# Kernel optimization log

Measured on AMD Instinct MI355X. Metric: run time of the kernel, lower is better.

The kernel has to match this reference:

```python
import jax, jax.numpy as jnp
import numpy as np
from jax import lax

B, L, D, H = 2, 4096, 1024, 16
K = 4            # short conv kernel size
HD = D // H      # head dim = 64
EPS = 1e-5


def causal_dw_conv(x, w):
    # depthwise causal conv: x [B,L,D], w [D,K]
    xp = jnp.pad(x, ((0, 0), (K - 1, 0), (0, 0)))
    out = xp[:, 0:L, :] * w[:, 0]
    for j in range(1, K):
        out = out + xp[:, j:j + L, :] * w[:, j]
    return out


def setup_inputs() -> dict:
    key = jax.random.key(0)
    ks = jax.random.split(key, 10)
    s = 0.02
    return {
        "hidden_states": jax.random.normal(ks[0], (B, L, D), jnp.float32),
        "Wq": jax.random.normal(ks[1], (D, D), jnp.float32) * s,
        "Wk": jax.random.normal(ks[2], (D, D), jnp.float32) * s,
        "Wv": jax.random.normal(ks[3], (D, D), jnp.float32) * s,
        "Wb": jax.random.normal(ks[4], (D, H), jnp.float32) * s,
        "conv_q": jax.random.normal(ks[5], (D, K), jnp.float32) * s,
        "conv_k": jax.random.normal(ks[6], (D, K), jnp.float32) * s,
        "conv_v": jax.random.normal(ks[7], (D, K), jnp.float32) * s,
        "o_norm_w": jnp.ones((HD,), jnp.float32),
        "Wo": jax.random.normal(ks[8], (D, D), jnp.float32) * s,
    }


def reference(hidden_states, Wq, Wk, Wv, Wb, conv_q, conv_k, conv_v, o_norm_w, Wo):
    x = hidden_states
    # projections + short causal conv with SiLU (qk_activation == 'silu')
    q = jax.nn.silu(causal_dw_conv(x @ Wq, conv_q))
    k = jax.nn.silu(causal_dw_conv(x @ Wk, conv_k))
    v = jax.nn.silu(causal_dw_conv(x @ Wv, conv_v))

    # [B,L,D] -> [L,B,H,hd] for the time scan
    def to_heads(t):
        return t.reshape(B, L, H, HD).transpose(1, 0, 2, 3)

    q, k, v = to_heads(q), to_heads(k), to_heads(v)

    # l2 qk-norm
    q = q / jnp.linalg.norm(q, axis=-1, keepdims=True)
    k = k / jnp.linalg.norm(k, axis=-1, keepdims=True)

    # beta gate [L,B,H]
    beta = jax.nn.sigmoid(x @ Wb).transpose(1, 0, 2)

    def step(S, inp):
        qt, kt, vt, bt = inp  # [B,H,hd] x3, [B,H]
        v_old = jnp.einsum('bhk,bhkv->bhv', kt, S)
        delta = (vt - v_old) * bt[..., None]
        S = S + jnp.einsum('bhk,bhv->bhkv', kt, delta)
        ot = jnp.einsum('bhk,bhkv->bhv', qt, S)
        return S, ot

    S0 = jnp.zeros((B, H, HD, HD), x.dtype)
    _, o = lax.scan(step, S0, (q, k, v, beta))  # o: [L,B,H,hd]
    o = o.transpose(1, 0, 2, 3)  # [B,L,H,hd]

    # per-head RMSNorm
    rms = jax.lax.rsqrt(jnp.mean(o * o, axis=-1, keepdims=True) + EPS)
    o = o * rms * o_norm_w

    return o.reshape(B, L, D) @ Wo
```

## Files before the change

kernel.cpp:

```cpp
#include <hip/hip_runtime.h>
#include <hip/hip_bf16.h>
#include <math.h>

#define BB 2
#define LL 4096
#define DD 1024
#define HH 16
#define HDIM 64
#define CC 64
#define NC 64
#define BH 32
#define GG 8
#define GS 8

typedef __attribute__((ext_vector_type(8))) short short8;
typedef __attribute__((ext_vector_type(4))) float f32x4;
typedef unsigned short u16;
typedef unsigned int u32;

__device__ __forceinline__ u16 f2bf(float f) {
    unsigned int u = __float_as_uint(f);
    unsigned int r = (u + 0x7fffu + ((u >> 16) & 1u)) >> 16;
    return (u16)r;
}
__device__ __forceinline__ float bf2f(u16 h) {
    return __uint_as_float((unsigned)h << 16);
}
__device__ __forceinline__ void split2(float x, u16& h, u16& l) {
    h = f2bf(x);
    l = f2bf(x - bf2f(h));
}
__device__ __forceinline__ u32 packhl(float x) {
    u16 h, l; split2(x, h, l);
    return (u32)h | ((u32)l << 16);
}
__device__ __forceinline__ float unpackhl(u32 v) {
    return bf2f((u16)v) + bf2f((u16)(v >> 16));
}
__device__ __forceinline__ float4 ld_bf4(const u16* p) {
    uint2 v = *(const uint2*)p;
    return make_float4(bf2f((u16)v.x), bf2f((u16)(v.x >> 16)),
                       bf2f((u16)v.y), bf2f((u16)(v.y >> 16)));
}

__device__ __forceinline__ void gld_lds16(const void* g, void* l) {
    __builtin_amdgcn_global_load_lds(
        (const __attribute__((address_space(1))) void*)g,
        (__attribute__((address_space(3))) void*)l, 16, 0, 0);
}

__device__ __forceinline__ int swz(int r, int c) {
    return (r << 6) + ((((c >> 2) ^ (r >> 2)) & 15) << 2) + (c & 3);
}
__device__ __forceinline__ int swze(int r, int c) {
    return (r << 6) + (c ^ (((r ^ (r >> 3)) & 7) << 3));
}

__device__ __forceinline__ void mm64(const u16* __restrict__ Ah, const u16* __restrict__ Al,
                                     const u16* __restrict__ Bh, const u16* __restrict__ Bl,
                                     f32x4* acc, int w, int lane) {
    const int ln = lane & 15, kg = (lane >> 4) * 8;
#pragma unroll
    for (int kb = 0; kb < 2; ++kb) {
        const int k0 = kb * 32 + kg;
        short8 ah = *(const short8*)&Ah[swze(w * 16 + ln, k0)];
        short8 al = *(const short8*)&Al[swze(w * 16 + ln, k0)];
#pragma unroll
        for (int j = 0; j < 4; ++j) {
            short8 bh = *(const short8*)&Bh[swze(j * 16 + ln, k0)];
            short8 bl = *(const short8*)&Bl[swze(j * 16 + ln, k0)];
            acc[j] = __builtin_amdgcn_mfma_f32_16x16x32_bf16(ah, bh, acc[j], 0, 0, 0);
            acc[j] = __builtin_amdgcn_mfma_f32_16x16x32_bf16(ah, bl, acc[j], 0, 0, 0);
            acc[j] = __builtin_amdgcn_mfma_f32_16x16x32_bf16(al, bh, acc[j], 0, 0, 0);
        }
    }
}
__device__ __forceinline__ void mm64_bb(const u16* __restrict__ Ah,
                                        const u16* __restrict__ Bh,
                                        f32x4* acc, int w, int lane) {
    const int ln = lane & 15, kg = (lane >> 4) * 8;
#pragma unroll
    for (int kb = 0; kb < 2; ++kb) {
        const int k0 = kb * 32 + kg;
        short8 ah = *(const short8*)&Ah[swze(w * 16 + ln, k0)];
#pragma unroll
        for (int j = 0; j < 4; ++j) {
            short8 bh = *(const short8*)&Bh[swze(j * 16 + ln, k0)];
            acc[j] = __builtin_amdgcn_mfma_f32_16x16x32_bf16(ah, bh, acc[j], 0, 0, 0);
        }
    }
}
__device__ __forceinline__ void mm64_ab(const u16* __restrict__ Ah,
                                        const u16* __restrict__ Bh, const u16* __restrict__ Bl,
                                        f32x4* acc, int w, int lane) {
    const int ln = lane & 15, kg = (lane >> 4) * 8;
#pragma unroll
    for (int kb = 0; kb < 2; ++kb) {
        const int k0 = kb * 32 + kg;
        short8 ah = *(const short8*)&Ah[swze(w * 16 + ln, k0)];
#pragma unroll
        for (int j = 0; j < 4; ++j) {
            short8 bh = *(const short8*)&Bh[swze(j * 16 + ln, k0)];
            short8 bl = *(const short8*)&Bl[swze(j * 16 + ln, k0)];
            acc[j] = __builtin_amdgcn_mfma_f32_16x16x32_bf16(ah, bh, acc[j], 0, 0, 0);
            acc[j] = __builtin_amdgcn_mfma_f32_16x16x32_bf16(ah, bl, acc[j], 0, 0, 0);
        }
    }
}

__device__ __forceinline__ void g_to_ls(const float* __restrict__ G, u16* Ah, u16* Al, int tid) {
#pragma unroll
    for (int p = 0; p < 4; ++p) {
        int flat = p * 1024 + tid * 4;
        int r = flat >> 6, c = flat & 63;
        float4 v = *(const float4*)&G[flat];
        u16 h0, l0, h1, l1, h2, l2, h3, l3;
        split2(v.x, h0, l0); split2(v.y, h1, l1);
        split2(v.z, h2, l2); split2(v.w, h3, l3);
        int idx = swze(r, c);
        uint2 hv, lv;
        hv.x = (unsigned)h0 | ((unsigned)h1 << 16); hv.y = (unsigned)h2 | ((unsigned)h3 << 16);
        lv.x = (unsigned)l0 | ((unsigned)l1 << 16); lv.y = (unsigned)l2 | ((unsigned)l3 << 16);
        *(uint2*)&Ah[idx] = hv;
        *(uint2*)&Al[idx] = lv;
    }
}
__device__ __forceinline__ void g_to_ls_b(const u16* __restrict__ G16, u16* Ah, int tid) {
#pragma unroll
    for (int p = 0; p < 2; ++p) {
        int flat = p * 2048 + tid * 8;
        int r = flat >> 6, c = flat & 63;
        *(short8*)&Ah[swze(r, c)] = *(const short8*)&G16[flat];
    }
}

__device__ __forceinline__ void pload(uint4 pf[4], const u32* __restrict__ G, int tid) {
    pf[0] = *(const uint4*)&G[tid * 8];
    pf[1] = *(const uint4*)&G[tid * 8 + 4];
    pf[2] = *(const uint4*)&G[2048 + tid * 8];
    pf[3] = *(const uint4*)&G[2048 + tid * 8 + 4];
}
__device__ __forceinline__ void pstore_ls(const uint4 pf[4], u16* Ah, u16* Al, int tid) {
#pragma unroll
    for (int p = 0; p < 2; ++p) {
        int flat = p * 2048 + tid * 8;
        int r = flat >> 6, c = flat & 63;
        uint4 a = pf[2 * p], b = pf[2 * p + 1];
        short8 hi, lo;
        hi[0] = (short)(u16)a.x; hi[1] = (short)(u16)a.y;
        hi[2] = (short)(u16)a.z; hi[3] = (short)(u16)a.w;
        hi[4] = (short)(u16)b.x; hi[5] = (short)(u16)b.y;
        hi[6] = (short)(u16)b.z; hi[7] = (short)(u16)b.w;
        lo[0] = (short)(a.x >> 16); lo[1] = (short)(a.y >> 16);
        lo[2] = (short)(a.z >> 16); lo[3] = (short)(a.w >> 16);
        lo[4] = (short)(b.x >> 16); lo[5] = (short)(b.y >> 16);
        lo[6] = (short)(b.z >> 16); lo[7] = (short)(b.w >> 16);
        *(short8*)&Ah[swze(r, c)] = hi;
        *(short8*)&Al[swze(r, c)] = lo;
    }
}
__device__ __forceinline__ void gp_to_ls(const u32* __restrict__ G, u16* Ah, u16* Al, int tid) {
    uint4 pf[4];
    pload(pf, G, tid);
    pstore_ls(pf, Ah, Al, tid);
}

__device__ __forceinline__ void frag_to_ls(const f32x4* acc, u16* Ah, u16* Al, int w, int lane) {
    const int g = lane >> 4, ln = lane & 15;
#pragma unroll
    for (int j = 0; j < 4; ++j)
#pragma unroll
        for (int r = 0; r < 4; ++r) {
            int row = w * 16 + g * 4 + r, col = j * 16 + ln;
            u16 h, l; split2(acc[j][r], h, l);
            Ah[swze(row, col)] = h;
            Al[swze(row, col)] = l;
        }
}

__device__ __forceinline__ void gp_to_frag(const u32* __restrict__ G, f32x4* acc, int w, int lane) {
    const int g = lane >> 4, ln = lane & 15;
#pragma unroll
    for (int j = 0; j < 4; ++j)
#pragma unroll
        for (int r = 0; r < 4; ++r)
            acc[j][r] = unpackhl(G[(w * 16 + g * 4 + r) * 64 + j * 16 + ln]);
}
__device__ __forceinline__ void gp_add_frag(const u32* __restrict__ G, f32x4* acc, int w, int lane) {
    const int g = lane >> 4, ln = lane & 15;
#pragma unroll
    for (int j = 0; j < 4; ++j)
#pragma unroll
        for (int r = 0; r < 4; ++r)
            acc[j][r] += unpackhl(G[(w * 16 + g * 4 + r) * 64 + j * 16 + ln]);
}
__device__ __forceinline__ void frag_to_gp(const f32x4* acc, u32* __restrict__ G, int w, int lane) {
    const int g = lane >> 4, ln = lane & 15;
#pragma unroll
    for (int j = 0; j < 4; ++j)
#pragma unroll
        for (int r = 0; r < 4; ++r)
            G[(w * 16 + g * 4 + r) * 64 + j * 16 + ln] = packhl(acc[j][r]);
}

__global__ __launch_bounds__(256) void cast_bf16_k(const float* __restrict__ in,
                                                   u16* __restrict__ out) {
    int i = (blockIdx.x * 256 + threadIdx.x) * 8;
    float4 a = *(const float4*)&in[i];
    float4 b = *(const float4*)&in[i + 4];
    uint4 o;
    o.x = (unsigned)f2bf(a.x) | ((unsigned)f2bf(a.y) << 16);
    o.y = (unsigned)f2bf(a.z) | ((unsigned)f2bf(a.w) << 16);
    o.z = (unsigned)f2bf(b.x) | ((unsigned)f2bf(b.y) << 16);
    o.w = (unsigned)f2bf(b.z) | ((unsigned)f2bf(b.w) << 16);
    *(uint4*)&out[i] = o;
}

__global__ __launch_bounds__(256) void transW4_k(const float* __restrict__ W0,
                                                 const float* __restrict__ W1,
                                                 const float* __restrict__ W2,
                                                 const float* __restrict__ W3,
                                                 u16* __restrict__ WT0) {
    __shared__ float t[32][33];
    const int which = blockIdx.z;
    const float* W = (which == 0) ? W0 : (which == 1) ? W1 : (which == 2) ? W2 : W3;
    u16* WT = WT0 + (size_t)which * 1048576;
    const int bx = blockIdx.x * 32, by = blockIdx.y * 32;
#pragma unroll
    for (int p = 0; p < 4; ++p) {
        int idx = p * 256 + threadIdx.x;
        int r = idx >> 5, cc = idx & 31;
        t[r][cc] = W[(size_t)(by + r) * 1024 + bx + cc];
    }
    __syncthreads();
#pragma unroll
    for (int p = 0; p < 4; ++p) {
        int idx = p * 256 + threadIdx.x;
        int r = idx >> 5, cc = idx & 31;
        WT[(size_t)(bx + r) * 1024 + by + cc] = f2bf(t[cc][r]);
    }
}

__device__ __forceinline__ void gemm_core256(const u16* A, const u16* BT,
                                             int m0, int n0, f32x4 acc[8][4]) {
    __shared__ __align__(16) short As[4][256 * 32];
    __shared__ __align__(16) short Bs[4][256 * 32];
    const int tid = threadIdx.x;
    const int lane = tid & 63, w = tid >> 6;
    const int wr = w >> 2, wc = w & 3;
    const int ln15 = lane & 15, kch = lane >> 4;
    const int erow = tid >> 2;
    const int ecol = (((tid & 3) ^ ((tid >> 3) & 3)) << 3);

#define STAGE256(buf, t)                                                      \
    {   const int k0_ = (t) * 32;                                             \
        _Pragma("unroll")                                                     \
        for (int rr = 0; rr < 2; ++rr) {                                      \
            gld_lds16(A  + (size_t)(m0 + rr * 128 + erow) * 1024 + k0_ + ecol,\
                      (short*)As[buf] + rr * 4096 + tid * 8);                 \
            gld_lds16(BT + (size_t)(n0 + rr * 128 + erow) * 1024 + k0_ + ecol,\
                      (short*)Bs[buf] + rr * 4096 + tid * 8);                 \
        } }

#define RF256(Fa, Fb, buf)                                                    \
    {   _Pragma("unroll")                                                     \
        for (int i = 0; i < 8; ++i) {                                         \
            int row = wr * 128 + i * 16 + ln15;                               \
            Fa[i] = *(const short8*)&As[buf][row * 32 + ((kch ^ ((row >> 1) & 3)) << 3)]; \
        }                                                                     \
        _Pragma("unroll")                                                     \
        for (int j = 0; j < 4; ++j) {                                         \
            int row = wc * 64 + j * 16 + ln15;                                \
            Fb[j] = *(const short8*)&Bs[buf][row * 32 + ((kch ^ ((row >> 1) & 3)) << 3)]; \
        } }

#define MM256(Fa, Fb)                                                         \
    {   __builtin_amdgcn_s_setprio(1);                                        \
        _Pragma("unroll")                                                     \
        for (int i = 0; i < 8; ++i)                                           \
            _Pragma("unroll")                                                 \
            for (int j = 0; j < 4; ++j)                                       \
                acc[i][j] = __builtin_amdgcn_mfma_f32_16x16x32_bf16(Fa[i], Fb[j], acc[i][j], 0, 0, 0); \
        __builtin_amdgcn_s_setprio(0); }

#define BODY256(t, Ca, Cb, Na, Nb)                                            \
    {   if ((t) + 3 < 32) STAGE256(((t) + 3) & 3, (t) + 3);                   \
        if ((t) < 29)       asm volatile("s_waitcnt vmcnt(8)" ::: "memory");  \
        else if ((t) == 29) asm volatile("s_waitcnt vmcnt(4)" ::: "memory");  \
        else if ((t) == 30) asm volatile("s_waitcnt vmcnt(0)" ::: "memory");  \
        asm volatile("s_waitcnt lgkmcnt(0)" ::: "memory");                    \
        __builtin_amdgcn_s_barrier();                                         \
        if ((t) < 31) RF256(Na, Nb, ((t) + 1) & 3);                           \
        MM256(Ca, Cb); }

    short8 Xa[8], Xb[4], Ya[8], Yb[4];
    STAGE256(0, 0);
    STAGE256(1, 1);
    STAGE256(2, 2);
    asm volatile("s_waitcnt vmcnt(8)" ::: "memory");
    __builtin_amdgcn_s_barrier();
    RF256(Xa, Xb, 0);
    for (int t2 = 0; t2 < 32; t2 += 2) {
        BODY256(t2, Xa, Xb, Ya, Yb);
        BODY256(t2 + 1, Ya, Yb, Xa, Xb);
    }
#undef STAGE256
#undef RF256
#undef MM256
#undef BODY256
}

__device__ __forceinline__ int xcd_swz(int lid, int nwg) {
    int q = nwg >> 3;
    return (lid & 7) * q + (lid >> 3);
}

__global__ __launch_bounds__(512, 2) void gemm_bf16(const u16* __restrict__ A,
                                                    const u16* __restrict__ BT,
                                                    float* __restrict__ C) {
    const int lid = blockIdx.y * 4 + blockIdx.x;
    const int sid = xcd_swz(lid, 128);
    const int m0 = (sid >> 2) * 256, n0 = (sid & 3) * 256;
    f32x4 acc[8][4] = {};
    gemm_core256(A, BT, m0, n0, acc);
    const int lane = threadIdx.x & 63, w = threadIdx.x >> 6;
    const int crow0 = m0 + (w >> 2) * 128 + (lane >> 4) * 4;
    const int ccol0 = n0 + (w & 3) * 64 + (lane & 15);
#pragma unroll
    for (int i = 0; i < 8; ++i)
#pragma unroll
        for (int j = 0; j < 4; ++j)
#pragma unroll
            for (int r = 0; r < 4; ++r)
                C[(size_t)(crow0 + i * 16 + r) * 1024 + ccol0 + j * 16] = acc[i][j][r];
}

__global__ __launch_bounds__(512, 2) void gemm_qkv(const u16* __restrict__ A,
                                                   const u16* __restrict__ WT0,
                                                   u16* __restrict__ xq16,
                                                   u16* __restrict__ xk16,
                                                   u16* __restrict__ xv16) {
    const int lid = blockIdx.y * 12 + blockIdx.x;
    const int sid = xcd_swz(lid, 384);
    const int lbx = sid % 12;
    const int which = lbx >> 2;
    const int n0 = (lbx & 3) * 256;
    const int m0 = (sid / 12) * 256;
    const u16* BT = WT0 + (size_t)which * 1048576;
    f32x4 acc[8][4] = {};
    gemm_core256(A, BT, m0, n0, acc);
    const int lane = threadIdx.x & 63, w = threadIdx.x >> 6;
    const int crow0 = m0 + (w >> 2) * 128 + (lane >> 4) * 4;
    const int ccol0 = n0 + (w & 3) * 64 + (lane & 15);
    u16* C16 = (which == 0) ? xq16 : (which == 1) ? xk16 : xv16;
#pragma unroll
    for (int i = 0; i < 8; ++i)
#pragma unroll
        for (int j = 0; j < 4; ++j)
#pragma unroll
            for (int r = 0; r < 4; ++r)
                C16[(size_t)(crow0 + i * 16 + r) * 1024 + ccol0 + j * 16] = f2bf(acc[i][j][r]);
}

__global__ __launch_bounds__(256) void beta_k(const float* __restrict__ X,
                                              const float* __restrict__ Wb,
                                              float* __restrict__ beta) {
    int idx = blockIdx.x * 256 + threadIdx.x;
    int row = idx >> 4, h = idx & 15;
    const float* xr = X + (size_t)row * DD;
    float s = 0.f;
    for (int k4 = 0; k4 < DD; k4 += 4) {
        float4 xv = *(const float4*)&xr[k4];
        s += xv.x * Wb[(k4 + 0) * HH + h];
        s += xv.y * Wb[(k4 + 1) * HH + h];
        s += xv.z * Wb[(k4 + 2) * HH + h];
        s += xv.w * Wb[(k4 + 3) * HH + h];
    }
    float bv = 1.f / (1.f + expf(-s));
    int b = row >> 12, l = row & (LL - 1);
    beta[((size_t)b * HH + h) * LL + l] = bv;
}

__global__ __launch_bounds__(256) void conv3_k(const u16* __restrict__ xq16,
                                               const u16* __restrict__ xk16,
                                               const u16* __restrict__ xv16,
                                               const float* __restrict__ cwq,
                                               const float* __restrict__ cwk,
                                               const float* __restrict__ cwv,
                                               u16* __restrict__ q16,
                                               u16* __restrict__ k16,
                                               u16* __restrict__ v16) {
    const int which = blockIdx.z;
    const float* cw = (which == 0) ? cwq : (which == 1) ? cwk : cwv;
    const int l0 = blockIdx.x * 16, b = blockIdx.y;
    const int tid = threadIdx.x;
    const int d0 = tid * 4;
    const float4 w0 = *(const float4*)&cw[(d0 + 0) * 4];
    const float4 w1 = *(const float4*)&cw[(d0 + 1) * 4];
    const float4 w2 = *(const float4*)&cw[(d0 + 2) * 4];
    const float4 w3 = *(const float4*)&cw[(d0 + 3) * 4];
    const int h = d0 >> 6, hd = d0 & 63;
    const u16* Xb = ((which == 0) ? xq16 : (which == 1) ? xk16 : xv16) + (size_t)b * LL * DD;
    u16* O16 = (which == 0) ? q16 : (which == 1) ? k16 : v16;
    float4 xm3 = make_float4(0, 0, 0, 0), xm2 = xm3, xm1 = xm3;
    if (l0 > 0) {
        xm3 = ld_bf4(&Xb[(size_t)(l0 - 3) * DD + d0]);
        xm2 = ld_bf4(&Xb[(size_t)(l0 - 2) * DD + d0]);
        xm1 = ld_bf4(&Xb[(size_t)(l0 - 1) * DD + d0]);
    }
#pragma unroll
    for (int t = 0; t < 16; ++t) {
        const int l = l0 + t;
        float4 xc = ld_bf4(&Xb[(size_t)l * DD + d0]);
        float a0 = xm3.x * w0.x + xm2.x * w0.y + xm1.x * w0.z + xc.x * w0.w;
        float a1 = xm3.y * w1.x + xm2.y * w1.y + xm1.y * w1.z + xc.y * w1.w;
        float a2 = xm3.z * w2.x + xm2.z * w2.y + xm1.z * w2.z + xc.z * w2.w;
        float a3 = xm3.w * w3.x + xm2.w * w3.y + xm1.w * w3.z + xc.w * w3.w;
        a0 = a0 / (1.f + expf(-a0));
        a1 = a1 / (1.f + expf(-a1));
        a2 = a2 / (1.f + expf(-a2));
        a3 = a3 / (1.f + expf(-a3));
        if (which < 2) {
            float s = a0 * a0 + a1 * a1 + a2 * a2 + a3 * a3;
            s += __shfl_xor(s, 1);
            s += __shfl_xor(s, 2);
            s += __shfl_xor(s, 4);
            s += __shfl_xor(s, 8);
            float sc = rsqrtf(s);
            a0 *= sc; a1 *= sc; a2 *= sc; a3 *= sc;
        }
        uint2 o;
        o.x = (unsigned)f2bf(a0) | ((unsigned)f2bf(a1) << 16);
        o.y = (unsigned)f2bf(a2) | ((unsigned)f2bf(a3) << 16);
        *(uint2*)&O16[(((size_t)b * HH + h) * LL + l) * 64 + hd] = o;
        xm3 = xm2; xm2 = xm1; xm1 = xc;
    }
}

__global__ __launch_bounds__(256) void phaseA6(const u16* __restrict__ kg16,
                                               const u16* __restrict__ vg16,
                                               const float* __restrict__ betag,
                                               u32* __restrict__ WgP,
                                               u32* __restrict__ UgTP,
                                               u32* __restrict__ PallP,
                                               u32* __restrict__ BallTP) {
    __shared__ __align__(16) char pool[73728];
    u16* Kh   = (u16*)pool;
    u16* KTh  = (u16*)(pool + 8192);
    float* At = (float*)(pool + 16384);
    float* WU = (float*)(pool + 32768);
    u16* WTh  = (u16*)pool;
    u16* WTl  = (u16*)(pool + 16384);
    u16* UTh  = (u16*)(pool + 24576);
    u16* UTl  = (u16*)(pool + 65536);
    float* scr = (float*)(pool + 32768);

    const int c = blockIdx.x, bh = blockIdx.y;
    const int tid = threadIdx.x, lane = tid & 63, w = tid >> 6;
    const int g = lane >> 4, ln = lane & 15;
    const int t0 = (tid >> 4) * 4, d4 = (tid & 15) * 4;
    const size_t base = ((size_t)bh * LL + (size_t)c * 64) * 64;
    const size_t obase = ((size_t)bh * NC + c) * 4096;
    const float* bet = betag + (size_t)bh * LL + (size_t)c * 64;

    g_to_ls_b(kg16 + base, Kh, tid);
    {
        u16 kv[4][4];
#pragma unroll
        for (int i = 0; i < 4; ++i) {
            uint2 v = *(const uint2*)&kg16[base + (size_t)(t0 + i) * 64 + d4];
            kv[i][0] = (u16)v.x; kv[i][1] = (u16)(v.x >> 16);
            kv[i][2] = (u16)v.y; kv[i][3] = (u16)(v.y >> 16);
        }
#pragma unroll
        for (int j = 0; j < 4; ++j) {
            uint2 hv;
            hv.x = (unsigned)kv[0][j] | ((unsigned)kv[1][j] << 16);
            hv.y = (unsigned)kv[2][j] | ((unsigned)kv[3][j] << 16);
            *(uint2*)&KTh[swze(d4 + j, t0)] = hv;
        }
    }
    __syncthreads();
    {
        f32x4 acc[4] = {};
        mm64_bb(Kh, Kh, acc, w, lane);
#pragma unroll
        for (int r = 0; r < 4; ++r) {
            int t = w * 16 + g * 4 + r;
            float bt = bet[t];
#pragma unroll
            for (int j = 0; j < 4; ++j) {
                int s = j * 16 + ln;
                At[t * 64 + s] = (s < t) ? bt * acc[j][r] : 0.f;
            }
        }
    }
#pragma unroll
    for (int p = 0; p < 8; ++p) {
        int flat = p * 1024 + tid * 4;
        int t = flat >> 7, j = flat & 127;
        float bt = bet[t];
        float4 src;
        if (j < 64) src = ld_bf4(&Kh[swze(t, j)]);
        else        src = ld_bf4(&vg16[base + (size_t)t * 64 + (j - 64)]);
        src.x *= bt; src.y *= bt; src.z *= bt; src.w *= bt;
        *(float4*)&WU[t * 128 + j] = src;
    }
    __syncthreads();
#pragma unroll
    for (int pb = 0; pb < 4; ++pb) {
        const int r0 = pb * 16;
        if (pb > 0) {
            const int col = tid & 127;
            const int rbase = r0 + (tid >> 7) * 8;
            float acc8[8] = {};
            for (int r = 0; r < r0; r += 4) {
                float u0 = WU[(r + 0) * 128 + col], u1 = WU[(r + 1) * 128 + col];
                float u2 = WU[(r + 2) * 128 + col], u3 = WU[(r + 3) * 128 + col];
#pragma unroll
                for (int i = 0; i < 8; ++i) {
                    float4 a4 = *(const float4*)&At[(rbase + i) * 64 + r];
                    acc8[i] += a4.x * u0 + a4.y * u1 + a4.z * u2 + a4.w * u3;
                }
            }
#pragma unroll
            for (int i = 0; i < 8; ++i) WU[(rbase + i) * 128 + col] -= acc8[i];
            __syncthreads();
        }
        if (tid < 128) {
            const int col = tid;
            float wv[16];
            wv[0] = WU[r0 * 128 + col];
#pragma unroll
            for (int t = 1; t < 16; ++t) {
                float a = WU[(r0 + t) * 128 + col];
#pragma unroll
                for (int r = 0; r < t; ++r) a -= At[(r0 + t) * 64 + r0 + r] * wv[r];
                wv[t] = a;
            }
#pragma unroll
            for (int t = 1; t < 16; ++t) WU[(r0 + t) * 128 + col] = wv[t];
        }
        __syncthreads();
    }
#pragma unroll
    for (int p = 0; p < 4; ++p) {
        int flat = p * 1024 + tid * 4;
        int t = flat >> 6, j = flat & 63;
        float4 v = *(const float4*)&WU[t * 128 + j];
        uint4 o;
        o.x = packhl(v.x); o.y = packhl(v.y); o.z = packhl(v.z); o.w = packhl(v.w);
        *(uint4*)&WgP[obase + flat] = o;
    }
    {
        u16 h4[4][4], l4[4][4];
#pragma unroll
        for (int i = 0; i < 4; ++i) {
            float4 v = *(const float4*)&WU[(t0 + i) * 128 + d4];
            split2(v.x, h4[i][0], l4[i][0]); split2(v.y, h4[i][1], l4[i][1]);
            split2(v.z, h4[i][2], l4[i][2]); split2(v.w, h4[i][3], l4[i][3]);
        }
#pragma unroll
        for (int j = 0; j < 4; ++j) {
            uint2 hv, lv;
            hv.x = (unsigned)h4[0][j] | ((unsigned)h4[1][j] << 16);
            hv.y = (unsigned)h4[2][j] | ((unsigned)h4[3][j] << 16);
            lv.x = (unsigned)l4[0][j] | ((unsigned)l4[1][j] << 16);
            lv.y = (unsigned)l4[2][j] | ((unsigned)l4[3][j] << 16);
            *(uint2*)&WTh[swze(d4 + j, t0)] = hv;
            *(uint2*)&WTl[swze(d4 + j, t0)] = lv;
        }
#pragma unroll
        for (int i = 0; i < 4; ++i) {
            float4 v = *(const float4*)&WU[(t0 + i) * 128 + 64 + d4];
            split2(v.x, h4[i][0], l4[i][0]); split2(v.y, h4[i][1], l4[i][1]);
            split2(v.z, h4[i][2], l4[i][2]); split2(v.w, h4[i][3], l4[i][3]);
        }
#pragma unroll
        for (int j = 0; j < 4; ++j) {
            uint2 hv, lv;
            hv.x = (unsigned)h4[0][j] | ((unsigned)h4[1][j] << 16);
            hv.y = (unsigned)h4[2][j] | ((unsigned)h4[3][j] << 16);
            lv.x = (unsigned)l4[0][j] | ((unsigned)l4[1][j] << 16);
            lv.y = (unsigned)l4[2][j] | ((unsigned)l4[3][j] << 16);
            *(uint2*)&UTh[swze(d4 + j, t0)] = hv;
            *(uint2*)&UTl[swze(d4 + j, t0)] = lv;
        }
    }
    __syncthreads();
#pragma unroll
    for (int p = 0; p < 4; ++p) {
        int flat = p * 1024 + tid * 4;
        int n = flat >> 6, tt = flat & 63;
        int idx = swze(n, tt);
        uint2 hh = *(const uint2*)&UTh[idx];
        uint2 ll2 = *(const uint2*)&UTl[idx];
        uint4 o;
        o.x = (hh.x & 0xffffu) | (ll2.x << 16);
        o.y = (hh.x >> 16) | (ll2.x & 0xffff0000u);
        o.z = (hh.y & 0xffffu) | (ll2.y << 16);
        o.w = (hh.y >> 16) | (ll2.y & 0xffff0000u);
        *(uint4*)&UgTP[obase + flat] = o;
    }
    f32x4 aP[4] = {}, aB[4] = {};
    mm64_ab(KTh, WTh, WTl, aP, w, lane);
    mm64_ab(KTh, UTh, UTl, aB, w, lane);
#pragma unroll
    for (int j = 0; j < 4; ++j)
#pragma unroll
        for (int r = 0; r < 4; ++r) {
            int row = w * 16 + g * 4 + r, col = j * 16 + ln;
            float pv = ((row == col) ? 1.f : 0.f) - aP[j][r];
            PallP[obase + (size_t)row * 64 + col] = packhl(pv);
            scr[swz(row, col)] = aB[j][r];
        }
    __syncthreads();
#pragma unroll
    for (int p = 0; p < 4; ++p) {
        int flat = p * 1024 + tid * 4;
        int n = flat >> 6, dd = flat & 63;
        uint4 o;
        o.x = packhl(scr[swz(dd + 0, n)]);
        o.y = packhl(scr[swz(dd + 1, n)]);
        o.z = packhl(scr[swz(dd + 2, n)]);
        o.w = packhl(scr[swz(dd + 3, n)]);
        *(uint4*)&BallTP[obase + flat] = o;
    }
}

__global__ __launch_bounds__(256) void compose4(const u32* __restrict__ PallP,
                                                const u32* __restrict__ BallTP,
                                                u32* __restrict__ PgP,
                                                u32* __restrict__ BgTP) {
    __shared__ __align__(16) char pool[81920];
    u16* Ph = (u16*)pool;
    u16* Pl = (u16*)(pool + 8192);
    u16* Bh = (u16*)(pool + 16384);
    u16* Bl = (u16*)(pool + 24576);
    u16* nh = (u16*)(pool + 32768);
    u16* nl = (u16*)(pool + 40960);
    float* scr = (float*)(pool + 49152);
    const int g = blockIdx.x, bh = blockIdx.y;
    const int tid = threadIdx.x, lane = tid & 63, w = tid >> 6;
    const int gi = lane >> 4, ln = lane & 15;
    const size_t base0 = ((size_t)bh * NC + (size_t)g * GS) * 4096;
    f32x4 mP[4], mB[4];
#pragma unroll
    for (int p = 0; p < 4; ++p) {
        int flat = p * 1024 + tid * 4;
        int r = flat >> 6, c4 = flat & 63;
        uint4 pk = *(const uint4*)&PallP[base0 + flat];
        *(float4*)&scr[swz(r, c4)] =
            make_float4(unpackhl(pk.x), unpackhl(pk.y), unpackhl(pk.z), unpackhl(pk.w));
    }
    gp_to_frag(BallTP + base0, mB, w, lane);
    __syncthreads();
#pragma unroll
    for (int j = 0; j < 4; ++j)
#pragma unroll
        for (int r = 0; r < 4; ++r) {
            int row = w * 16 + gi * 4 + r, col = j * 16 + ln;
            mP[j][r] = scr[swz(col, row)];
        }
    uint4 pf[4];
    pload(pf, PallP + base0 + 4096, tid);
    for (int s = 1; s < GS; ++s) {
        __syncthreads();
        frag_to_ls(mP, Ph, Pl, w, lane);
        frag_to_ls(mB, Bh, Bl, w, lane);
        pstore_ls(pf, nh, nl, tid);
        __syncthreads();
        if (s < GS - 1) pload(pf, PallP + base0 + (size_t)(s + 1) * 4096, tid);
        f32x4 aP[4] = {}, aB[4] = {};
        mm64(Ph, Pl, nh, nl, aP, w, lane);
        mm64(Bh, Bl, nh, nl, aB, w, lane);
        gp_add_frag(BallTP + base0 + (size_t)s * 4096, aB, w, lane);
#pragma unroll
        for (int j = 0; j < 4; ++j) { mP[j] = aP[j]; mB[j] = aB[j]; }
    }
    const size_t gbase = ((size_t)bh * GG + g) * 4096;
    frag_to_gp(mB, BgTP + gbase, w, lane);
    __syncthreads();
#pragma unroll
    for (int j = 0; j < 4; ++j)
#pragma unroll
        for (int r = 0; r < 4; ++r) {
            int row = w * 16 + gi * 4 + r, col = j * 16 + ln;
            scr[swz(row, col)] = mP[j][r];
        }
    __syncthreads();
#pragma unroll
    for (int p = 0; p < 4; ++p) {
        int flat = p * 1024 + tid * 4;
        int a = flat >> 6, b0 = flat & 63;
        uint4 o;
        o.x = packhl(scr[swz(b0 + 0, a)]);
        o.y = packhl(scr[swz(b0 + 1, a)]);
        o.z = packhl(scr[swz(b0 + 2, a)]);
        o.w = packhl(scr[swz(b0 + 3, a)]);
        *(uint4*)&PgP[gbase + flat] = o;
    }
}

__global__ __launch_bounds__(256) void scanG4(const u32* __restrict__ PgP,
                                              const u32* __restrict__ BgTP,
                                              u32* __restrict__ SallTP) {
    __shared__ __align__(16) char pool[32768];
    u16* Sh = (u16*)pool;
    u16* Sl = (u16*)(pool + 8192);
    u16* nh = (u16*)(pool + 16384);
    u16* nl = (u16*)(pool + 24576);
    const int bh = blockIdx.x;
    const int tid = threadIdx.x, lane = tid & 63, w = tid >> 6;
    f32x4 mS[4] = {};
    for (int g = 0; g < GG; ++g) {
        const size_t sbase = ((size_t)bh * NC + (size_t)g * GS) * 4096;
        frag_to_gp(mS, SallTP + sbase, w, lane);
        if (g == GG - 1) break;
        __syncthreads();
        frag_to_ls(mS, Sh, Sl, w, lane);
        gp_to_ls(PgP + ((size_t)bh * GG + g) * 4096, nh, nl, tid);
        __syncthreads();
        f32x4 a[4] = {};
        mm64(Sh, Sl, nh, nl, a, w, lane);
        gp_add_frag(BgTP + ((size_t)bh * GG + g) * 4096, a, w, lane);
#pragma unroll
        for (int j = 0; j < 4; ++j) mS[j] = a[j];
    }
}

__global__ __launch_bounds__(256) void rollout4(const u32* __restrict__ PallP,
                                                const u32* __restrict__ BallTP,
                                                u32* __restrict__ SallTP) {
    __shared__ __align__(16) char pool[32768];
    u16* Sh = (u16*)pool;
    u16* Sl = (u16*)(pool + 8192);
    u16* nh = (u16*)(pool + 16384);
    u16* nl = (u16*)(pool + 24576);
    const int g = blockIdx.x, bh = blockIdx.y;
    const int tid = threadIdx.x, lane = tid & 63, w = tid >> 6;
    const size_t base0 = ((size_t)bh * NC + (size_t)g * GS) * 4096;
    f32x4 mS[4];
    gp_to_frag(SallTP + base0, mS, w, lane);
    uint4 pf[4];
    pload(pf, PallP + base0, tid);
    for (int j = 1; j < GS; ++j) {
        __syncthreads();
        frag_to_ls(mS, Sh, Sl, w, lane);
        pstore_ls(pf, nh, nl, tid);
        __syncthreads();
        if (j < GS - 1) pload(pf, PallP + base0 + (size_t)j * 4096, tid);
        f32x4 a[4] = {};
        mm64(Sh, Sl, nh, nl, a, w, lane);
        gp_add_frag(BallTP + base0 + (size_t)(j - 1) * 4096, a, w, lane);
#pragma unroll
        for (int jj = 0; jj < 4; ++jj) mS[jj] = a[jj];
        frag_to_gp(mS, SallTP + base0 + (size_t)j * 4096, w, lane);
    }
}

__global__ __launch_bounds__(256) void phaseO5(const u32* __restrict__ WgP,
                                               const u32* __restrict__ UgTP,
                                               const u16* __restrict__ qg16,
                                               const u16* __restrict__ kg16,
                                               const u32* __restrict__ SallTP,
                                               const float* __restrict__ nw,
                                               u16* __restrict__ ob) {
    __shared__ __align__(16) char pool[57344];
    u16* Qh = (u16*)pool;
    u16* Kh = (u16*)(pool + 8192);
    u16* Wh = (u16*)(pool + 16384);
    u16* Wl = (u16*)(pool + 24576);
    u16* Sh = (u16*)(pool + 32768);
    u16* Sl = (u16*)(pool + 40960);
    u16* Dl = (u16*)(pool + 49152);
    u16* Dh = Kh;
    u16* Mh = Wh; u16* Ml = Wl;
    const int c = blockIdx.x, bh = blockIdx.y;
    const int b = bh >> 4, h = bh & 15;
    const int tid = threadIdx.x, lane = tid & 63, w = tid >> 6;
    const int gi = lane >> 4, ln = lane & 15;
    const size_t tbase = ((size_t)bh * NC + c) * 4096;
    const size_t qkbase = ((size_t)bh * LL + (size_t)c * 64) * 64;
    g_to_ls_b(qg16 + qkbase, Qh, tid);
    g_to_ls_b(kg16 + qkbase, Kh, tid);
    gp_to_ls(WgP + tbase, Wh, Wl, tid);
    gp_to_ls(SallTP + tbase, Sh, Sl, tid);
    __syncthreads();
    f32x4 aM[4] = {}, aD[4] = {};
    mm64_bb(Qh, Kh, aM, w, lane);
    mm64(Sh, Sl, Wh, Wl, aD, w, lane);
    __syncthreads();
#pragma unroll
    for (int j = 0; j < 4; ++j)
#pragma unroll
        for (int r = 0; r < 4; ++r) {
            int row = w * 16 + gi * 4 + r, col = j * 16 + ln;
            float mv = (col <= row) ? aM[j][r] : 0.f;
            u16 mh_, ml_; split2(mv, mh_, ml_);
            Mh[swze(row, col)] = mh_;
            Ml[swze(row, col)] = ml_;
            float dv = unpackhl(UgTP[tbase + (size_t)row * 64 + col]) - aD[j][r];
            u16 dh_, dl_; split2(dv, dh_, dl_);
            Dh[swze(row, col)] = dh_;
            Dl[swze(row, col)] = dl_;
        }
    __syncthreads();
    f32x4 aO[4] = {};
    mm64_ab(Qh, Sh, Sl, aO, w, lane);
    mm64(Mh, Ml, Dh, Dl, aO, w, lane);
    float nwv[4];
#pragma unroll
    for (int j = 0; j < 4; ++j) nwv[j] = nw[j * 16 + ln];
#pragma unroll
    for (int r = 0; r < 4; ++r) {
        float ss = 0.f;
#pragma unroll
        for (int j = 0; j < 4; ++j) ss += aO[j][r] * aO[j][r];
        ss += __shfl_xor(ss, 1);
        ss += __shfl_xor(ss, 2);
        ss += __shfl_xor(ss, 4);
        ss += __shfl_xor(ss, 8);
        float rms = rsqrtf(ss * (1.f / 64.f) + 1e-5f);
        int row = w * 16 + gi * 4 + r;
        size_t orow = ((size_t)b * LL + (size_t)c * 64 + row) * DD + (size_t)h * 64;
#pragma unroll
        for (int j = 0; j < 4; ++j)
            ob[orow + j * 16 + ln] = f2bf(aO[j][r] * rms * nwv[j]);
    }
}

extern "C" void kernel_launch(void* const* d_in, const int* in_sizes, int n_in,
                              void* d_out, int out_size, void* d_ws, size_t ws_size,
                              hipStream_t stream) {
    const float* x  = (const float*)d_in[0];
    const float* Wq = (const float*)d_in[1];
    const float* Wk = (const float*)d_in[2];
    const float* Wv = (const float*)d_in[3];
    const float* Wb = (const float*)d_in[4];
    const float* cq = (const float*)d_in[5];
    const float* ck = (const float*)d_in[6];
    const float* cv = (const float*)d_in[7];
    const float* nw = (const float*)d_in[8];
    const float* Wo = (const float*)d_in[9];
    float* out = (float*)d_out;
    float* ws = (float*)d_ws;

    const size_t SZ = (size_t)BB * LL * DD;
    u16* xv16    = (u16*)ws;
    u16* v16     = (u16*)(ws + SZ);
    u32* WgP     = (u32*)(ws + 2 * SZ);
    u32* UgTP    = (u32*)(ws + 3 * SZ);
    u32* SallTP  = (u32*)(ws + 4 * SZ);
    u16* xb   = (u16*)(ws + 5 * SZ);
    u16* q16  = xb;
    u16* xq16 = (u16*)(ws + 5 * SZ) + SZ;
    u16* xk16 = (u16*)(ws + 5 * SZ) + 2 * SZ;
    u16* k16  = (u16*)(ws + 5 * SZ) + 3 * SZ;
    float* beta = ws + 7 * SZ;
    u16* wqT  = (u16*)(beta + (size_t)BH * LL);
    u32* PgP  = (u32*)(wqT + (size_t)4 * 1048576);
    u32* BgTP = PgP + 1048576;

    u32* PallP  = (u32*)ws;
    u32* BallTP = (u32*)out;
    u16* ob   = (u16*)(ws + SZ);
    u16* woT  = wqT + (size_t)3 * 1048576;

    dim3 blk(256);

    cast_bf16_k<<<dim3(4096), blk, 0, stream>>>(x, xb);
    transW4_k<<<dim3(32, 32, 4), blk, 0, stream>>>(Wq, Wk, Wv, Wo, wqT);
    gemm_qkv<<<dim3(12, 32), dim3(512), 0, stream>>>(xb, wqT, xq16, xk16, xv16);
    beta_k<<<dim3(512), blk, 0, stream>>>(x, Wb, beta);
    conv3_k<<<dim3(LL / 16, BB, 3), blk, 0, stream>>>(xq16, xk16, xv16, cq, ck, cv, q16, k16, v16);
    phaseA6<<<dim3(NC, BH), blk, 0, stream>>>(k16, v16, beta, WgP, UgTP, PallP, BallTP);
    compose4<<<dim3(GG, BH), blk, 0, stream>>>(PallP, BallTP, PgP, BgTP);
    scanG4<<<dim3(BH), blk, 0, stream>>>(PgP, BgTP, SallTP);
    rollout4<<<dim3(GG, BH), blk, 0, stream>>>(PallP, BallTP, SallTP);
    phaseO5<<<dim3(NC, BH), blk, 0, stream>>>(WgP, UgTP, q16, k16, SallTP, nw, ob);
    gemm_bf16<<<dim3(4, 32), dim3(512), 0, stream>>>(ob, woT, out);
}
```

Baseline: 352.2 us.

## Fuse causal conv into chunk phase kernels and merge prep kernels

Removes the standalone conv3_k kernel. The causal depthwise conv, SiLU and L2 norm are now computed on the fly inside phaseA7 (for k and v) and phaseO7 (for q and k), reading the pre-conv projections directly. The goal is to avoid writing and re-reading the q16/k16/v16 intermediates and to save a launch. The k conv is done twice, once in each phase, and each tile reads 3 halo rows. The bf16 cast and weight-transpose kernels are also merged into a single prep_k launch.

```diff
diff --git a/kernel.cpp b/kernel.cpp
--- a/kernel.cpp
+++ b/kernel.cpp
@@ -105,32 +105,6 @@
             acc[j] = __builtin_amdgcn_mfma_f32_16x16x32_bf16(ah, bh, acc[j], 0, 0, 0);
             acc[j] = __builtin_amdgcn_mfma_f32_16x16x32_bf16(ah, bl, acc[j], 0, 0, 0);
         }
-    }
-}
-
-__device__ __forceinline__ void g_to_ls(const float* __restrict__ G, u16* Ah, u16* Al, int tid) {
-#pragma unroll
-    for (int p = 0; p < 4; ++p) {
-        int flat = p * 1024 + tid * 4;
-        int r = flat >> 6, c = flat & 63;
-        float4 v = *(const float4*)&G[flat];
-        u16 h0, l0, h1, l1, h2, l2, h3, l3;
-        split2(v.x, h0, l0); split2(v.y, h1, l1);
-        split2(v.z, h2, l2); split2(v.w, h3, l3);
-        int idx = swze(r, c);
-        uint2 hv, lv;
-        hv.x = (unsigned)h0 | ((unsigned)h1 << 16); hv.y = (unsigned)h2 | ((unsigned)h3 << 16);
-        lv.x = (unsigned)l0 | ((unsigned)l1 << 16); lv.y = (unsigned)l2 | ((unsigned)l3 << 16);
-        *(uint2*)&Ah[idx] = hv;
-        *(uint2*)&Al[idx] = lv;
-    }
-}
-__device__ __forceinline__ void g_to_ls_b(const u16* __restrict__ G16, u16* Ah, int tid) {
-#pragma unroll
-    for (int p = 0; p < 2; ++p) {
-        int flat = p * 2048 + tid * 8;
-        int r = flat >> 6, c = flat & 63;
-        *(short8*)&Ah[swze(r, c)] = *(const short8*)&G16[flat];
     }
 }
 
@@ -203,29 +177,70 @@
             G[(w * 16 + g * 4 + r) * 64 + j * 16 + ln] = packhl(acc[j][r]);
 }
 
-__global__ __launch_bounds__(256) void cast_bf16_k(const float* __restrict__ in,
-                                                   u16* __restrict__ out) {
-    int i = (blockIdx.x * 256 + threadIdx.x) * 8;
-    float4 a = *(const float4*)&in[i];
-    float4 b = *(const float4*)&in[i + 4];
-    uint4 o;
-    o.x = (unsigned)f2bf(a.x) | ((unsigned)f2bf(a.y) << 16);
-    o.y = (unsigned)f2bf(a.z) | ((unsigned)f2bf(a.w) << 16);
-    o.z = (unsigned)f2bf(b.x) | ((unsigned)f2bf(b.y) << 16);
-    o.w = (unsigned)f2bf(b.z) | ((unsigned)f2bf(b.w) << 16);
-    *(uint4*)&out[i] = o;
-}
-
-__global__ __launch_bounds__(256) void transW4_k(const float* __restrict__ W0,
-                                                 const float* __restrict__ W1,
-                                                 const float* __restrict__ W2,
-                                                 const float* __restrict__ W3,
-                                                 u16* __restrict__ WT0) {
+__device__ __forceinline__ void conv_tile(const u16* __restrict__ X, const float* __restrict__ cw,
+                                          int b, int c, int h, int rg4, int cg4,
+                                          bool norm, u16 kb[4][4]) {
+    const float4 w0 = *(const float4*)&cw[(h * 64 + cg4 + 0) * 4];
+    const float4 w1 = *(const float4*)&cw[(h * 64 + cg4 + 1) * 4];
+    const float4 w2 = *(const float4*)&cw[(h * 64 + cg4 + 2) * 4];
+    const float4 w3 = *(const float4*)&cw[(h * 64 + cg4 + 3) * 4];
+    float4 xin[7];
+#pragma unroll
+    for (int i = 0; i < 7; ++i) {
+        int l = c * 64 + rg4 - 3 + i;
+        xin[i] = (l >= 0) ? ld_bf4(&X[((size_t)b * LL + l) * DD + h * 64 + cg4])
+                          : make_float4(0.f, 0.f, 0.f, 0.f);
+    }
+#pragma unroll
+    for (int i = 0; i < 4; ++i) {
+        float a0 = xin[i].x * w0.x + xin[i + 1].x * w0.y + xin[i + 2].x * w0.z + xin[i + 3].x * w0.w;
+        float a1 = xin[i].y * w1.x + xin[i + 1].y * w1.y + xin[i + 2].y * w1.z + xin[i + 3].y * w1.w;
+        float a2 = xin[i].z * w2.x + xin[i + 1].z * w2.y + xin[i + 2].z * w2.z + xin[i + 3].z * w2.w;
+        float a3 = xin[i].w * w3.x + xin[i + 1].w * w3.y + xin[i + 2].w * w3.z + xin[i + 3].w * w3.w;
+        a0 = a0 / (1.f + expf(-a0));
+        a1 = a1 / (1.f + expf(-a1));
+        a2 = a2 / (1.f + expf(-a2));
+        a3 = a3 / (1.f + expf(-a3));
+        if (norm) {
+            float s = a0 * a0 + a1 * a1 + a2 * a2 + a3 * a3;
+            s += __shfl_xor(s, 1);
+            s += __shfl_xor(s, 2);
+            s += __shfl_xor(s, 4);
+            s += __shfl_xor(s, 8);
+            float sc = rsqrtf(s);
+            a0 *= sc; a1 *= sc; a2 *= sc; a3 *= sc;
+        }
+        kb[i][0] = f2bf(a0); kb[i][1] = f2bf(a1);
+        kb[i][2] = f2bf(a2); kb[i][3] = f2bf(a3);
+    }
+}
+
+__global__ __launch_bounds__(256) void prep_k(const float* __restrict__ in,
+                                              u16* __restrict__ out,
+                                              const float* __restrict__ W0,
+                                              const float* __restrict__ W1,
+                                              const float* __restrict__ W2,
+                                              const float* __restrict__ W3,
+                                              u16* __restrict__ WT0) {
     __shared__ float t[32][33];
-    const int which = blockIdx.z;
+    const int bid = blockIdx.x;
+    if (bid < 4096) {
+        int i = (bid * 256 + threadIdx.x) * 8;
+        float4 a = *(const float4*)&in[i];
+        float4 b = *(const float4*)&in[i + 4];
+        uint4 o;
+        o.x = (unsigned)f2bf(a.x) | ((unsigned)f2bf(a.y) << 16);
+        o.y = (unsigned)f2bf(a.z) | ((unsigned)f2bf(a.w) << 16);
+        o.z = (unsigned)f2bf(b.x) | ((unsigned)f2bf(b.y) << 16);
+        o.w = (unsigned)f2bf(b.z) | ((unsigned)f2bf(b.w) << 16);
+        *(uint4*)&out[i] = o;
+        return;
+    }
+    const int t2 = bid - 4096;
+    const int which = t2 >> 10, rem = t2 & 1023;
+    const int bx = (rem & 31) * 32, by = (rem >> 5) * 32;
     const float* W = (which == 0) ? W0 : (which == 1) ? W1 : (which == 2) ? W2 : W3;
     u16* WT = WT0 + (size_t)which * 1048576;
-    const int bx = blockIdx.x * 32, by = blockIdx.y * 32;
 #pragma unroll
     for (int p = 0; p < 4; ++p) {
         int idx = p * 256 + threadIdx.x;
@@ -381,65 +396,11 @@
     beta[((size_t)b * HH + h) * LL + l] = bv;
 }
 
-__global__ __launch_bounds__(256) void conv3_k(const u16* __restrict__ xq16,
-                                               const u16* __restrict__ xk16,
+__global__ __launch_bounds__(256) void phaseA7(const u16* __restrict__ xk16,
                                                const u16* __restrict__ xv16,
-                                               const float* __restrict__ cwq,
+                                               const float* __restrict__ betag,
                                                const float* __restrict__ cwk,
                                                const float* __restrict__ cwv,
-                                               u16* __restrict__ q16,
-                                               u16* __restrict__ k16,
-                                               u16* __restrict__ v16) {
-    const int which = blockIdx.z;
-    const float* cw = (which == 0) ? cwq : (which == 1) ? cwk : cwv;
-    const int l0 = blockIdx.x * 16, b = blockIdx.y;
-    const int tid = threadIdx.x;
-    const int d0 = tid * 4;
-    const float4 w0 = *(const float4*)&cw[(d0 + 0) * 4];
-    const float4 w1 = *(const float4*)&cw[(d0 + 1) * 4];
-    const float4 w2 = *(const float4*)&cw[(d0 + 2) * 4];
-    const float4 w3 = *(const float4*)&cw[(d0 + 3) * 4];
-    const int h = d0 >> 6, hd = d0 & 63;
-    const u16* Xb = ((which == 0) ? xq16 : (which == 1) ? xk16 : xv16) + (size_t)b * LL * DD;
-    u16* O16 = (which == 0) ? q16 : (which == 1) ? k16 : v16;
-    float4 xm3 = make_float4(0, 0, 0, 0), xm2 = xm3, xm1 = xm3;
-    if (l0 > 0) {
-        xm3 = ld_bf4(&Xb[(size_t)(l0 - 3) * DD + d0]);
-        xm2 = ld_bf4(&Xb[(size_t)(l0 - 2) * DD + d0]);
-        xm1 = ld_bf4(&Xb[(size_t)(l0 - 1) * DD + d0]);
-    }
-#pragma unroll
-    for (int t = 0; t < 16; ++t) {
-        const int l = l0 + t;
-        float4 xc = ld_bf4(&Xb[(size_t)l * DD + d0]);
-        float a0 = xm3.x * w0.x + xm2.x * w0.y + xm1.x * w0.z + xc.x * w0.w;
-        float a1 = xm3.y * w1.x + xm2.y * w1.y + xm1.y * w1.z + xc.y * w1.w;
-        float a2 = xm3.z * w2.x + xm2.z * w2.y + xm1.z * w2.z + xc.z * w2.w;
-        float a3 = xm3.w * w3.x + xm2.w * w3.y + xm1.w * w3.z + xc.w * w3.w;
-        a0 = a0 / (1.f + expf(-a0));
-        a1 = a1 / (1.f + expf(-a1));
-        a2 = a2 / (1.f + expf(-a2));
-        a3 = a3 / (1.f + expf(-a3));
-        if (which < 2) {
-            float s = a0 * a0 + a1 * a1 + a2 * a2 + a3 * a3;
-            s += __shfl_xor(s, 1);
-            s += __shfl_xor(s, 2);
-            s += __shfl_xor(s, 4);
-            s += __shfl_xor(s, 8);
-            float sc = rsqrtf(s);
-            a0 *= sc; a1 *= sc; a2 *= sc; a3 *= sc;
-        }
-        uint2 o;
-        o.x = (unsigned)f2bf(a0) | ((unsigned)f2bf(a1) << 16);
-        o.y = (unsigned)f2bf(a2) | ((unsigned)f2bf(a3) << 16);
-        *(uint2*)&O16[(((size_t)b * HH + h) * LL + l) * 64 + hd] = o;
-        xm3 = xm2; xm2 = xm1; xm1 = xc;
-    }
-}
-
-__global__ __launch_bounds__(256) void phaseA6(const u16* __restrict__ kg16,
-                                               const u16* __restrict__ vg16,
-                                               const float* __restrict__ betag,
                                                u32* __restrict__ WgP,
                                                u32* __restrict__ UgTP,
                                                u32* __restrict__ PallP,
@@ -453,31 +414,42 @@
     u16* WTl  = (u16*)(pool + 16384);
     u16* UTh  = (u16*)(pool + 24576);
     u16* UTl  = (u16*)(pool + 65536);
+    u16* Vh   = (u16*)(pool + 65536);
     float* scr = (float*)(pool + 32768);
 
     const int c = blockIdx.x, bh = blockIdx.y;
+    const int b = bh >> 4, h = bh & 15;
     const int tid = threadIdx.x, lane = tid & 63, w = tid >> 6;
     const int g = lane >> 4, ln = lane & 15;
     const int t0 = (tid >> 4) * 4, d4 = (tid & 15) * 4;
-    const size_t base = ((size_t)bh * LL + (size_t)c * 64) * 64;
     const size_t obase = ((size_t)bh * NC + c) * 4096;
     const float* bet = betag + (size_t)bh * LL + (size_t)c * 64;
 
-    g_to_ls_b(kg16 + base, Kh, tid);
     {
-        u16 kv[4][4];
+        u16 kb[4][4];
+        conv_tile(xk16, cwk, b, c, h, t0, d4, true, kb);
 #pragma unroll
         for (int i = 0; i < 4; ++i) {
-            uint2 v = *(const uint2*)&kg16[base + (size_t)(t0 + i) * 64 + d4];
-            kv[i][0] = (u16)v.x; kv[i][1] = (u16)(v.x >> 16);
-            kv[i][2] = (u16)v.y; kv[i][3] = (u16)(v.y >> 16);
+            uint2 kp;
+            kp.x = (unsigned)kb[i][0] | ((unsigned)kb[i][1] << 16);
+            kp.y = (unsigned)kb[i][2] | ((unsigned)kb[i][3] << 16);
+            *(uint2*)&Kh[swze(t0 + i, d4)] = kp;
         }
 #pragma unroll
         for (int j = 0; j < 4; ++j) {
-            uint2 hv;
-            hv.x = (unsigned)kv[0][j] | ((unsigned)kv[1][j] << 16);
-            hv.y = (unsigned)kv[2][j] | ((unsigned)kv[3][j] << 16);
-            *(uint2*)&KTh[swze(d4 + j, t0)] = hv;
+            uint2 kt;
+            kt.x = (unsigned)kb[0][j] | ((unsigned)kb[1][j] << 16);
+            kt.y = (unsigned)kb[2][j] | ((unsigned)kb[3][j] << 16);
+            *(uint2*)&KTh[swze(d4 + j, t0)] = kt;
+        }
+        u16 vb[4][4];
+        conv_tile(xv16, cwv, b, c, h, t0, d4, false, vb);
+#pragma unroll
+        for (int i = 0; i < 4; ++i) {
+            uint2 vp;
+            vp.x = (unsigned)vb[i][0] | ((unsigned)vb[i][1] << 16);
+            vp.y = (unsigned)vb[i][2] | ((unsigned)vb[i][3] << 16);
+            *(uint2*)&Vh[swze(t0 + i, d4)] = vp;
         }
     }
     __syncthreads();
@@ -502,7 +474,7 @@
         float bt = bet[t];
         float4 src;
         if (j < 64) src = ld_bf4(&Kh[swze(t, j)]);
-        else        src = ld_bf4(&vg16[base + (size_t)t * 64 + (j - 64)]);
+        else        src = ld_bf4(&Vh[swze(t, j - 64)]);
         src.x *= bt; src.y *= bt; src.z *= bt; src.w *= bt;
         *(float4*)&WU[t * 128 + j] = src;
     }
@@ -759,11 +731,13 @@
     }
 }
 
-__global__ __launch_bounds__(256) void phaseO5(const u32* __restrict__ WgP,
+__global__ __launch_bounds__(256) void phaseO7(const u32* __restrict__ WgP,
                                                const u32* __restrict__ UgTP,
-                                               const u16* __restrict__ qg16,
-                                               const u16* __restrict__ kg16,
+                                               const u16* __restrict__ xq16,
+                                               const u16* __restrict__ xk16,
                                                const u32* __restrict__ SallTP,
+                                               const float* __restrict__ cwq,
+                                               const float* __restrict__ cwk,
                                                const float* __restrict__ nw,
                                                u16* __restrict__ ob) {
     __shared__ __align__(16) char pool[57344];
@@ -780,10 +754,28 @@
     const int b = bh >> 4, h = bh & 15;
     const int tid = threadIdx.x, lane = tid & 63, w = tid >> 6;
     const int gi = lane >> 4, ln = lane & 15;
+    const int t0 = (tid >> 4) * 4, d4 = (tid & 15) * 4;
     const size_t tbase = ((size_t)bh * NC + c) * 4096;
-    const size_t qkbase = ((size_t)bh * LL + (size_t)c * 64) * 64;
-    g_to_ls_b(qg16 + qkbase, Qh, tid);
-    g_to_ls_b(kg16 + qkbase, Kh, tid);
+    {
+        u16 qb[4][4];
+        conv_tile(xq16, cwq, b, c, h, t0, d4, true, qb);
+#pragma unroll
+        for (int i = 0; i < 4; ++i) {
+            uint2 qp;
+            qp.x = (unsigned)qb[i][0] | ((unsigned)qb[i][1] << 16);
+            qp.y = (unsigned)qb[i][2] | ((unsigned)qb[i][3] << 16);
+            *(uint2*)&Qh[swze(t0 + i, d4)] = qp;
+        }
+        u16 kb[4][4];
+        conv_tile(xk16, cwk, b, c, h, t0, d4, true, kb);
+#pragma unroll
+        for (int i = 0; i < 4; ++i) {
+            uint2 kp;
+            kp.x = (unsigned)kb[i][0] | ((unsigned)kb[i][1] << 16);
+            kp.y = (unsigned)kb[i][2] | ((unsigned)kb[i][3] << 16);
+            *(uint2*)&Kh[swze(t0 + i, d4)] = kp;
+        }
+    }
     gp_to_ls(WgP + tbase, Wh, Wl, tid);
     gp_to_ls(SallTP + tbase, Sh, Sl, tid);
     __syncthreads();
@@ -848,36 +840,33 @@
 
     const size_t SZ = (size_t)BB * LL * DD;
     u16* xv16    = (u16*)ws;
-    u16* v16     = (u16*)(ws + SZ);
+    u32* PallP   = (u32*)(ws + SZ);
     u32* WgP     = (u32*)(ws + 2 * SZ);
     u32* UgTP    = (u32*)(ws + 3 * SZ);
     u32* SallTP  = (u32*)(ws + 4 * SZ);
     u16* xb   = (u16*)(ws + 5 * SZ);
-    u16* q16  = xb;
     u16* xq16 = (u16*)(ws + 5 * SZ) + SZ;
     u16* xk16 = (u16*)(ws + 5 * SZ) + 2 * SZ;
-    u16* k16  = (u16*)(ws + 5 * SZ) + 3 * SZ;
     float* beta = ws + 7 * SZ;
     u16* wqT  = (u16*)(beta + (size_t)BH * LL);
     u32* PgP  = (u32*)(wqT + (size_t)4 * 1048576);
     u32* BgTP = PgP + 1048576;
 
-    u32* PallP  = (u32*)ws;
     u32* BallTP = (u32*)out;
     u16* ob   = (u16*)(ws + SZ);
     u16* woT  = wqT + (size_t)3 * 1048576;
 
     dim3 blk(256);
 
-    cast_bf16_k<<<dim3(4096), blk, 0, stream>>>(x, xb);
-    transW4_k<<<dim3(32, 32, 4), blk, 0, stream>>>(Wq, Wk, Wv, Wo, wqT);
+    prep_k<<<dim3(8192), blk, 0, stream>>>(x, xb, Wq, Wk, Wv, Wo, wqT);
     gemm_qkv<<<dim3(12, 32), dim3(512), 0, stream>>>(xb, wqT, xq16, xk16, xv16);
     beta_k<<<dim3(512), blk, 0, stream>>>(x, Wb, beta);
-    conv3_k<<<dim3(LL / 16, BB, 3), blk, 0, stream>>>(xq16, xk16, xv16, cq, ck, cv, q16, k16, v16);
-    phaseA6<<<dim3(NC, BH), blk, 0, stream>>>(k16, v16, beta, WgP, UgTP, PallP, BallTP);
+    phaseA7<<<dim3(NC, BH), blk, 0, stream>>>(xk16, xv16, beta, ck, cv,
+                                              WgP, UgTP, PallP, BallTP);
     compose4<<<dim3(GG, BH), blk, 0, stream>>>(PallP, BallTP, PgP, BgTP);
     scanG4<<<dim3(BH), blk, 0, stream>>>(PgP, BgTP, SallTP);
     rollout4<<<dim3(GG, BH), blk, 0, stream>>>(PallP, BallTP, SallTP);
-    phaseO5<<<dim3(NC, BH), blk, 0, stream>>>(WgP, UgTP, q16, k16, SallTP, nw, ob);
+    phaseO7<<<dim3(NC, BH), blk, 0, stream>>>(WgP, UgTP, xq16, xk16, SallTP,
+                                              cq, ck, nw, ob);
     gemm_bf16<<<dim3(4, 32), dim3(512), 0, stream>>>(ob, woT, out);
 }
```

After: 357.7 us. No clear change (+1.6%).
